# Kernel tuning notes

Measured on AMD Instinct MI355X. Metric: run time of the kernel, lower is better.

The kernel has to match this reference:

```python
import jax, jax.numpy as jnp
import numpy as np

C_FINE, C_MID, C_COARSE = 100, 20, 5
EPS = 1e-12


def setup_inputs() -> dict:
    key = jax.random.key(0)
    k1, k2 = jax.random.split(key)
    N, D = 262144, 128
    representations = jax.random.normal(k1, (N, D), dtype=jnp.float32)
    target_fine = jax.random.randint(k2, (N,), 0, C_FINE, dtype=jnp.int32)
    # nested hierarchy: fine -> mid (5 fines per mid), fine -> coarse (20 fines per coarse)
    fine2mid = (jnp.arange(C_FINE, dtype=jnp.int32) // (C_FINE // C_MID)).astype(jnp.int32)
    fine2coarse = (jnp.arange(C_FINE, dtype=jnp.int32) // (C_FINE // C_COARSE)).astype(jnp.int32)
    return {
        "representations": representations,
        "target_fine": target_fine,
        "fine2mid": fine2mid,
        "fine2coarse": fine2coarse,
    }


def _safe_norm(diff):
    # L2 norm along last axis; eps gives a 0 subgradient at diff==0
    return jnp.sqrt(jnp.sum(diff * diff, axis=-1) + EPS)


def _segment_mean(x, ids, num_segments):
    ones = jnp.ones(x.shape[:1], x.dtype)
    s = jax.ops.segment_sum(x, ids, num_segments=num_segments)
    c = jax.ops.segment_sum(ones, ids, num_segments=num_segments)
    return s / jnp.maximum(c, 1.0)[:, None]


def reference(representations, target_fine, fine2mid, fine2coarse):
    # ---- tree construction (vectorized version of the per-class Python loops) ----
    # fine prototypes: mean of representations per fine class  [C_FINE, D]
    fine_protos = _segment_mean(representations, target_fine, C_FINE)
    # mid prototypes: mean of child fine prototypes  [C_MID, D]
    mid_protos = _segment_mean(fine_protos, fine2mid, C_MID)
    # coarse prototypes: mean of child mid prototypes  [C_COARSE, D]
    mid2coarse = jax.ops.segment_max(fine2coarse, fine2mid, num_segments=C_MID)
    coarse_protos = _segment_mean(mid_protos, mid2coarse, C_COARSE)
    # (the root node contributes ||root - root|| = 0 to every pair, so it is omitted)

    # ---- pairwise tree-path distances over all fine-class pairs ----
    iu, ju = np.triu_indices(C_FINE, k=1)  # static C*(C-1)/2 = 4950 pairs
    ci, cj = fine2coarse[iu], fine2coarse[ju]
    mi, mj = fine2mid[iu], fine2mid[ju]
    tree_d = _safe_norm(coarse_protos[ci] - coarse_protos[cj]) \
           + _safe_norm(mid_protos[mi] - mid_protos[mj])
    # Euclidean distances between fine prototypes
    proto_d = _safe_norm(fine_protos[iu] - fine_protos[ju])

    # ---- CPCC: loss = 1 - Pearson correlation(tree_d, proto_d) ----
    tc = tree_d - jnp.mean(tree_d)
    pc = proto_d - jnp.mean(proto_d)
    corr = jnp.sum(tc * pc) / jnp.sqrt(jnp.sum(tc * tc) * jnp.sum(pc * pc) + EPS)
    return 1.0 - corr
```

## Files before the change

kernel.cpp:

```cpp
#include <hip/hip_runtime.h>
#include <math.h>

#define C_FINE   100
#define C_MID    20
#define C_COARSE 5
#define D        128
#define NROWS    262144
#define NPAIRS   4950
#define NBLK4    78

#define NB       512
#define ROWS_PB  (NROWS/NB)
#define NSTEP    (ROWS_PB/32)
#define MT       7
#define PSTR2    (113*128)

#define FP_OFF    0
#define DM_OFF    12800
#define DC_OFF    13200
#define ACC_OFF   13232
#define DONE_OFF  13244
#define CNT_OFF   13248
#define FSUM_OFF  13376
#define PART_OFF  26176

typedef __attribute__((ext_vector_type(8))) short bf16x8;
typedef __attribute__((ext_vector_type(4))) float f32x4;

static __device__ __forceinline__ unsigned short f2bf(float f) {
    unsigned int x = __float_as_uint(f);
    x += 0x7FFF + ((x >> 16) & 1);
    return (unsigned short)(x >> 16);
}

__global__ __launch_bounds__(512, 4) void kMF(const float* __restrict__ rep,
                                              const int* __restrict__ tgt,
                                              float* __restrict__ ws) {
    __shared__ float tile[2][32 * 128];
    __shared__ int   ltgt[ROWS_PB];
    __shared__ int   hist[128];
    const int t  = threadIdx.x;
    const int w  = t >> 6;
    const int l  = t & 63;
    const int lg = l >> 4;
    const int ll = l & 15;
    const int blk   = blockIdx.x;
    const int rbase = blk * ROWS_PB;

    if (t < 128) hist[t] = 0;
    __syncthreads();
    {
        int c = tgt[rbase + t];
        ltgt[t] = c;
        atomicAdd(&hist[c], 1);
    }

    const float4* rep4 = (const float4*)rep;
    const int tile4base = rbase * (D / 4);

    f32x4 acc[MT];
    #pragma unroll
    for (int m = 0; m < MT; ++m)
        #pragma unroll
        for (int i = 0; i < 4; ++i) acc[m][i] = 0.f;

    {
        float4 a0 = rep4[tile4base + t];
        float4 a1 = rep4[tile4base + 512 + t];
        ((float4*)tile[0])[t]       = a0;
        ((float4*)tile[0])[t + 512] = a1;
    }
    __syncthreads();

    #pragma unroll 1
    for (int s = 0; s < NSTEP; ++s) {
        const int buf = s & 1;
        float4 na, nb;
        if (s + 1 < NSTEP) {
            na = rep4[tile4base + (s + 1) * 1024 + t];
            nb = rep4[tile4base + (s + 1) * 1024 + 512 + t];
        }

        const float* tf = tile[buf];
        float vB[8];
        int   tv[8];
        #pragma unroll
        for (int j = 0; j < 8; ++j) {
            vB[j] = tf[(8 * lg + j) * D + 16 * w + ll];
            tv[j] = ltgt[s * 32 + 8 * lg + j];
        }
        bf16x8 b0;
        #pragma unroll
        for (int j = 0; j < 8; ++j) b0[j] = (short)f2bf(vB[j]);
        #pragma unroll
        for (int m = 0; m < MT; ++m) {
            const int cb = 16 * m + ll;
            bf16x8 a;
            #pragma unroll
            for (int j = 0; j < 8; ++j)
                a[j] = (tv[j] == cb) ? (short)0x3F80 : (short)0;
            acc[m] = __builtin_amdgcn_mfma_f32_16x16x32_bf16(a, b0, acc[m], 0, 0, 0);
        }

        if (s + 1 < NSTEP) {
            ((float4*)tile[buf ^ 1])[t]       = na;
            ((float4*)tile[buf ^ 1])[t + 512] = nb;
        }
        __syncthreads();
    }

    float* part = ws + PART_OFF + (size_t)blk * PSTR2;
    #pragma unroll
    for (int m = 0; m < MT; ++m)
        #pragma unroll
        for (int i = 0; i < 4; ++i)
            part[(16 * m + 4 * lg + i) * D + 16 * w + ll] = acc[m][i];
    if (t < 128) part[112 * D + t] = (t < C_FINE) ? (float)hist[t] : 0.f;
}

__global__ __launch_bounds__(512) void kRed(float* __restrict__ ws) {
    const int c = blockIdx.x;
    const int t = threadIdx.x;
    const int g = t >> 7, d = t & 127;
    float s = 0.f;
    #pragma unroll 8
    for (int b = g; b < NB; b += 4)
        s += ws[PART_OFF + (size_t)b * PSTR2 + c * D + d];
    __shared__ float red[4][128];
    red[g][d] = s;

    float cv = ws[PART_OFF + (size_t)t * PSTR2 + 112 * D + c];
    #pragma unroll
    for (int off = 32; off > 0; off >>= 1) cv += __shfl_down(cv, off);
    __shared__ float cw[8];
    if ((t & 63) == 0) cw[t >> 6] = cv;
    __syncthreads();
    if (g == 0) ws[FSUM_OFF + c * D + d] = red[0][d] + red[1][d] + red[2][d] + red[3][d];
    if (t == 0) {
        float tot = 0.f;
        #pragma unroll
        for (int q = 0; q < 8; ++q) tot += cw[q];
        ws[CNT_OFF + c] = tot;
    }
}

__global__ __launch_bounds__(256) void k3_hier(const int* __restrict__ f2m,
                                               const int* __restrict__ f2c,
                                               float* __restrict__ ws) {
    __shared__ float fineP[C_FINE][D];
    __shared__ float midP[C_MID][D + 1];
    __shared__ float coarP[C_COARSE][D + 1];
    __shared__ int   sf2m[C_FINE], sf2c[C_FINE], m2c[C_MID];
    __shared__ float midCnt[C_MID], coarCnt[C_COARSE];
    __shared__ float sTot[C_FINE];
    const int t = threadIdx.x;

    if (t < C_FINE) {
        sf2m[t] = f2m[t]; sf2c[t] = f2c[t];
        sTot[t] = ws[CNT_OFF + t];
    }
    for (int e = t; e < C_MID * (D + 1); e += 256) ((float*)midP)[e] = 0.f;
    for (int e = t; e < C_COARSE * (D + 1); e += 256) ((float*)coarP)[e] = 0.f;
    __syncthreads();

    for (int e = t; e < C_FINE * D; e += 256) {
        int c = e >> 7, d = e & 127;
        float v = ws[FSUM_OFF + e] / fmaxf(sTot[c], 1.f);
        fineP[c][d] = v;
        ws[FP_OFF + e] = v;
    }
    if (t < C_MID) {
        int cntv = 0, mx = -2147483647;
        for (int f = 0; f < C_FINE; ++f)
            if (sf2m[f] == t) { ++cntv; mx = max(mx, sf2c[f]); }
        midCnt[t] = (float)max(cntv, 1);
        m2c[t] = mx;
    }
    __syncthreads();

    if (t < D) {
        const int d = t;
        for (int f = 0; f < C_FINE; ++f)
            midP[sf2m[f]][d] += fineP[f][d];
        for (int m = 0; m < C_MID; ++m)
            midP[m][d] /= midCnt[m];
    }
    if (t >= 128 && t < 128 + C_COARSE) {
        int cc = t - 128, cntv = 0;
        for (int m = 0; m < C_MID; ++m) if (m2c[m] == cc) ++cntv;
        coarCnt[cc] = (float)max(cntv, 1);
    }
    __syncthreads();

    if (t < D) {
        const int d = t;
        for (int m = 0; m < C_MID; ++m)
            coarP[m2c[m]][d] += midP[m][d];
        for (int cc = 0; cc < C_COARSE; ++cc)
            coarP[cc][d] /= coarCnt[cc];
    }
    __syncthreads();

    for (int e = t; e < C_MID * C_MID; e += 256) {
        int m1 = e / C_MID, m2 = e % C_MID;
        float ss = 0.f;
        #pragma unroll 8
        for (int d = 0; d < D; ++d) {
            float df = midP[m1][d] - midP[m2][d];
            ss += df * df;
        }
        ws[DM_OFF + e] = sqrtf(ss + 1e-12f);
    }
    for (int e = t; e < C_COARSE * C_COARSE; e += 256) {
        int c1 = e / C_COARSE, c2 = e % C_COARSE;
        float ss = 0.f;
        #pragma unroll 8
        for (int d = 0; d < D; ++d) {
            float df = coarP[c1][d] - coarP[c2][d];
            ss += df * df;
        }
        ws[DC_OFF + e] = sqrtf(ss + 1e-12f);
    }
    if (t < 5) ((double*)(ws + ACC_OFF))[t] = 0.0;
    if (t == 5) ((int*)ws + DONE_OFF)[0] = 0;
}

__global__ __launch_bounds__(64) void k45_pairs(float* __restrict__ ws,
                                                const int* __restrict__ f2m,
                                                const int* __restrict__ f2c,
                                                float* __restrict__ out) {
    const int p = blockIdx.x * 64 + threadIdx.x;
    double st = 0, sp = 0, stp = 0, stt = 0, spp = 0;
    if (p < NPAIRS) {
        int i = 0, rem = p;
        while (rem >= C_FINE - 1 - i) { rem -= C_FINE - 1 - i; ++i; }
        int j = i + 1 + rem;

        const float4* Fi = (const float4*)(ws + FP_OFF + i * D);
        const float4* Fj = (const float4*)(ws + FP_OFF + j * D);
        float ss = 0.f;
        #pragma unroll
        for (int k = 0; k < D / 4; ++k) {
            float4 a = Fi[k], b = Fj[k];
            float dx = a.x - b.x, dy = a.y - b.y, dz = a.z - b.z, dw = a.w - b.w;
            ss += dx * dx + dy * dy + dz * dz + dw * dw;
        }
        float proto = sqrtf(ss + 1e-12f);
        float tree  = ws[DC_OFF + f2c[i] * C_COARSE + f2c[j]]
                    + ws[DM_OFF + f2m[i] * C_MID + f2m[j]];
        st = tree; sp = proto;
        stp = (double)tree * (double)proto;
        stt = (double)tree * (double)tree;
        spp = (double)proto * (double)proto;
    }
    for (int off = 32; off > 0; off >>= 1) {
        st  += __shfl_down(st, off);
        sp  += __shfl_down(sp, off);
        stp += __shfl_down(stp, off);
        stt += __shfl_down(stt, off);
        spp += __shfl_down(spp, off);
    }
    if (threadIdx.x == 0) {
        double* acc = (double*)(ws + ACC_OFF);
        atomicAdd(&acc[0], st);
        atomicAdd(&acc[1], sp);
        atomicAdd(&acc[2], stp);
        atomicAdd(&acc[3], stt);
        atomicAdd(&acc[4], spp);
        __threadfence();
        int* done = (int*)ws + DONE_OFF;
        int ticket = atomicAdd(done, 1);
        if (ticket == NBLK4 - 1) {
            double fst  = atomicAdd(&acc[0], 0.0);
            double fsp  = atomicAdd(&acc[1], 0.0);
            double fstp = atomicAdd(&acc[2], 0.0);
            double fstt = atomicAdd(&acc[3], 0.0);
            double fspp = atomicAdd(&acc[4], 0.0);
            const double n = (double)NPAIRS;
            double num = fstp - fst * fsp / n;
            double dtt = fstt - fst * fst / n;
            double dpp = fspp - fsp * fsp / n;
            double corr = num / sqrt(dtt * dpp + 1e-12);
            out[0] = (float)(1.0 - corr);
        }
    }
}

extern "C" void kernel_launch(void* const* d_in, const int* in_sizes, int n_in,
                              void* d_out, int out_size, void* d_ws, size_t ws_size,
                              hipStream_t stream) {
    const float* rep = (const float*)d_in[0];
    const int*   tgt = (const int*)d_in[1];
    const int*   f2m = (const int*)d_in[2];
    const int*   f2c = (const int*)d_in[3];
    float* ws  = (float*)d_ws;
    float* out = (float*)d_out;

    hipLaunchKernelGGL(kMF,       dim3(NB),     dim3(512), 0, stream, rep, tgt, ws);
    hipLaunchKernelGGL(kRed,      dim3(C_FINE), dim3(512), 0, stream, ws);
    hipLaunchKernelGGL(k3_hier,   dim3(1),      dim3(256), 0, stream, f2m, f2c, ws);
    hipLaunchKernelGGL(k45_pairs, dim3(NBLK4),  dim3(64),  0, stream,
                       ws, f2m, f2c, out);
}
```

Measured before the change: 86.38 us.

## Build one-hot A operand in LDS and swizzle tile layout to avoid bank conflicts

The per-step one-hot A matrix is no longer built in registers with 56 compares per thread. It is kept as a double-buffered bf16 image in shared memory, updated by clearing the previous step's entries and setting the next step's, and read with vector loads. The float tile is stored with an XOR swizzle on the float4 column so the strided B-fragment reads avoid LDS bank conflicts. The cost is extra LDS space (which may lower occupancy), extra shared-memory traffic, and more scattered stores in a 32-thread update.

```diff
diff --git a/kernel.cpp b/kernel.cpp
--- a/kernel.cpp
+++ b/kernel.cpp
@@ -37,6 +37,7 @@
                                               const int* __restrict__ tgt,
                                               float* __restrict__ ws) {
     __shared__ float tile[2][32 * 128];
+    __shared__ short Aimg[2][112 * 32];
     __shared__ int   ltgt[ROWS_PB];
     __shared__ int   hist[128];
     const int t  = threadIdx.x;
@@ -49,14 +50,25 @@
 
     if (t < 128) hist[t] = 0;
     __syncthreads();
-    {
-        int c = tgt[rbase + t];
-        ltgt[t] = c;
-        atomicAdd(&hist[c], 1);
-    }
 
     const float4* rep4 = (const float4*)rep;
     const int tile4base = rbase * (D / 4);
+
+    const int myc = tgt[rbase + t];
+    ltgt[t] = myc;
+    atomicAdd(&hist[myc], 1);
+    for (int e = t; e < 2 * 112 * 32 / 2; e += 512) ((int*)Aimg)[e] = 0;
+    {
+        float4 a0 = rep4[tile4base + t];
+        float4 a1 = rep4[tile4base + 512 + t];
+        const int r0 = t >> 5, d4 = t & 31;
+        const int r1 = 16 + r0;
+        ((float4*)tile[0])[r0 * 32 + (d4 ^ ((r0 >> 3) & 3))] = a0;
+        ((float4*)tile[0])[r1 * 32 + (d4 ^ ((r1 >> 3) & 3))] = a1;
+    }
+    __syncthreads();
+    if (t < 32) Aimg[0][myc * 32 + t] = (short)0x3F80;
+    __syncthreads();
 
     f32x4 acc[MT];
     #pragma unroll
@@ -64,13 +76,8 @@
         #pragma unroll
         for (int i = 0; i < 4; ++i) acc[m][i] = 0.f;
 
-    {
-        float4 a0 = rep4[tile4base + t];
-        float4 a1 = rep4[tile4base + 512 + t];
-        ((float4*)tile[0])[t]       = a0;
-        ((float4*)tile[0])[t + 512] = a1;
-    }
-    __syncthreads();
+    const int d4r = 4 * w + (ll >> 2);
+    const int bB  = lg * 1024 + ((d4r ^ lg) << 2) + (ll & 3);
 
     #pragma unroll 1
     for (int s = 0; s < NSTEP; ++s) {
@@ -82,29 +89,29 @@
         }
 
         const float* tf = tile[buf];
-        float vB[8];
-        int   tv[8];
-        #pragma unroll
-        for (int j = 0; j < 8; ++j) {
-            vB[j] = tf[(8 * lg + j) * D + 16 * w + ll];
-            tv[j] = ltgt[s * 32 + 8 * lg + j];
-        }
         bf16x8 b0;
         #pragma unroll
-        for (int j = 0; j < 8; ++j) b0[j] = (short)f2bf(vB[j]);
-        #pragma unroll
-        for (int m = 0; m < MT; ++m) {
-            const int cb = 16 * m + ll;
-            bf16x8 a;
-            #pragma unroll
-            for (int j = 0; j < 8; ++j)
-                a[j] = (tv[j] == cb) ? (short)0x3F80 : (short)0;
-            acc[m] = __builtin_amdgcn_mfma_f32_16x16x32_bf16(a, b0, acc[m], 0, 0, 0);
-        }
-
+        for (int j = 0; j < 8; ++j) b0[j] = (short)f2bf(tf[bB + j * 128]);
+
+        const short* Ab = Aimg[buf];
+        bf16x8 af[MT];
+        #pragma unroll
+        for (int m = 0; m < MT; ++m)
+            af[m] = *(const bf16x8*)&Ab[(16 * m + ll) * 32 + 8 * lg];
+        #pragma unroll
+        for (int m = 0; m < MT; ++m)
+            acc[m] = __builtin_amdgcn_mfma_f32_16x16x32_bf16(af[m], b0, acc[m], 0, 0, 0);
+
+        if (t < 32) {
+            short* An = (short*)Aimg[buf ^ 1];
+            if (s >= 1)        An[ltgt[(s - 1) * 32 + t] * 32 + t] = 0;
+            if (s + 1 < NSTEP) An[ltgt[(s + 1) * 32 + t] * 32 + t] = (short)0x3F80;
+        }
         if (s + 1 < NSTEP) {
-            ((float4*)tile[buf ^ 1])[t]       = na;
-            ((float4*)tile[buf ^ 1])[t + 512] = nb;
+            const int r0 = t >> 5, d4 = t & 31;
+            const int r1 = 16 + r0;
+            ((float4*)tile[buf ^ 1])[r0 * 32 + (d4 ^ ((r0 >> 3) & 3))] = na;
+            ((float4*)tile[buf ^ 1])[r1 * 32 + (d4 ^ ((r1 >> 3) & 3))] = nb;
         }
         __syncthreads();
     }
```

After: 81.70 us. 1.06x faster.
